# Performance work log

Measured on AMD Instinct MI355X. Metric: run time of the kernel, lower is better.

## Reference

```python
import jax, jax.numpy as jnp
import numpy as np

N_HEADS = 8
TOP_K = 2
EPS = 1e-5


def cross_node(x4, nf, tkv, Wq, bq, Wk, bk, Wv, bv, Wo, bo, gamma, beta, token_mask):
    # x4: [N, BL, 1, D]; nf: [N, BL, K, D]; tkv: [N, K, 1]; token_mask: [N] float (routed subset)
    N, BL, _, D = x4.shape
    K = nf.shape[2]
    H = N_HEADS
    dh = D // H
    nf = nf * tkv[:, None, :, :]  # use_weights: scale neighbors by topk similarity weights
    xf = x4.reshape(N * BL, D)
    nff = nf.reshape(N * BL, K, D)
    q = (xf @ Wq.T + bq).reshape(N * BL, H, dh)
    k = (nff @ Wk.T + bk).reshape(N * BL, K, H, dh)
    v = (nff @ Wv.T + bv).reshape(N * BL, K, H, dh)
    # flash_attn_func math: scaled dot-product over the K neighbors, per head
    scores = jnp.einsum('thd,tkhd->thk', q, k) / jnp.sqrt(jnp.asarray(dh, xf.dtype))
    attn = jax.nn.softmax(scores, axis=-1)
    o = jnp.einsum('thk,tkhd->thd', attn, v).reshape(N * BL, D)
    o = o @ Wo.T + bo
    # masked BatchNorm1d (training-mode batch stats over ONLY the gathered/routed tokens,
    # matching torch where each expert sees just its subset)
    m = jnp.broadcast_to(token_mask[:, None], (N, BL)).reshape(-1, 1)
    cnt = jnp.maximum(m.sum(), 1.0)
    mean = (o * m).sum(0) / cnt
    var = (((o - mean) ** 2) * m).sum(0) / cnt
    o = (o - mean) / jnp.sqrt(var + EPS) * gamma + beta
    return (o + xf).reshape(N, BL, D)


def moe_forward(x, mm, topk_values, Wr, br, eWq, eWk, eWv, eWo, ebq, ebk, ebv, ebo,
                eGamma, eBeta, eW1, eb1, mWq, mWk, mWv, mWo, mbq, mbk, mbv, mbo,
                mGamma, mBeta, mW2, mb2, topk_indices, modality_index):
    N, B, L, D = x.shape
    BL = B * L
    K = topk_indices.shape[1]
    E = Wr.shape[0]
    Mn = mWq.shape[0]
    # neighbor gather: nf[n, b*l, k] = x[topk_indices[n, k], b, l]
    nf = jnp.transpose(x[topk_indices], (0, 2, 3, 1, 4)).reshape(N, BL, K, D)
    x4 = x.reshape(N, BL, 1, D)
    tkv = topk_values.reshape(N, K, 1)
    # router softmax gating
    gate = jax.nn.softmax(mm.reshape(N, D) @ Wr.T + br, axis=-1)  # [N, E]
    _, te = jax.lax.top_k(gate, TOP_K)
    routed = jax.nn.one_hot(te, E, dtype=gate.dtype).sum(1)  # [N, E] 0/1
    f_i = routed.sum(0) / N
    P_i = gate.sum(0) / N
    balance_loss = E * jnp.sum(f_i * P_i)
    # capacity limiting via running cumsum per expert column
    keep = jnp.cumsum(routed, axis=0) <= (N / E)
    rprobs = gate * jnp.where(keep, routed, jnp.zeros_like(routed))
    active = rprobs.sum(-1) > 0  # [N]
    eprobs, eidx = jax.lax.top_k(rprobs, TOP_K)  # [N, TOP_K]
    # expert dispatch/combine (dense-masked equivalent of the per-expert gather/scatter)
    out_tok = jnp.zeros((N, BL, D), x.dtype)
    for i in range(E):
        sel = (eidx == i).any(-1) & active  # tokens gathered for expert i
        mask_f = sel.astype(x.dtype)
        prob_i = (eprobs * (eidx == i)).sum(-1)  # combine weight (0 for capacity-dropped)
        co = cross_node(x4, nf, tkv, eWq[i], ebq[i], eWk[i], ebk[i], eWv[i], ebv[i],
                        eWo[i], ebo[i], eGamma[i], eBeta[i], mask_f)
        co = co @ eW1[i].T + eb1[i]
        out_tok = out_tok + (mask_f * prob_i)[:, None, None] * co
    # modality experts: every token with modality m goes through modality expert m
    mod_out = jnp.zeros_like(out_tok)
    for m in range(Mn):
        mask_f = (modality_index[:, m, :] == 1).any(-1).astype(x.dtype)
        co = cross_node(x4, nf, tkv, mWq[m], mbq[m], mWk[m], mbk[m], mWv[m], mbv[m],
                        mWo[m], mbo[m], mGamma[m], mBeta[m], mask_f)
        co = co @ mW2[m].T + mb2[m]
        mod_out = mod_out + mask_f[:, None, None] * co
    out = (out_tok + mod_out / Mn).reshape(N, B, L, D)
    return out, balance_loss


def setup_inputs():
    key = jax.random.key(0)
    ks = jax.random.split(key, 7)
    N, B, L, D, K, E, Mn = 1024, 2, 8, 128, 16, 4, 4
    s = 1.0 / float(np.sqrt(D))
    inp = {}
    inp['x'] = jax.random.normal(ks[0], (N, B, L, D), jnp.float32)
    inp['mm'] = jax.random.normal(ks[1], (N, 1, D), jnp.float32)
    inp['topk_values'] = jax.random.uniform(ks[2], (N, K), jnp.float32)
    inp['topk_indices'] = jax.random.randint(ks[3], (N, K), 0, N, dtype=jnp.int32)
    inp['modality_index'] = jax.nn.one_hot(
        jax.random.randint(ks[4], (N,), 0, Mn, dtype=jnp.int32), Mn, dtype=jnp.int32
    ).reshape(N, Mn, 1)
    inp['Wr'] = jax.random.normal(ks[5], (E, D), jnp.float32) * s
    inp['br'] = jnp.zeros((E,), jnp.float32)
    kk = jax.random.split(ks[6], 10)
    for j, nm in enumerate(['eWq', 'eWk', 'eWv', 'eWo', 'eW1']):
        inp[nm] = jax.random.normal(kk[j], (E, D, D), jnp.float32) * s
    for j, nm in enumerate(['mWq', 'mWk', 'mWv', 'mWo', 'mW2']):
        inp[nm] = jax.random.normal(kk[5 + j], (Mn, D, D), jnp.float32) * s
    for nm in ['ebq', 'ebk', 'ebv', 'ebo', 'eBeta', 'eb1']:
        inp[nm] = jnp.zeros((E, D), jnp.float32)
    for nm in ['mbq', 'mbk', 'mbv', 'mbo', 'mBeta', 'mb2']:
        inp[nm] = jnp.zeros((Mn, D), jnp.float32)
    inp['eGamma'] = jnp.ones((E, D), jnp.float32)
    inp['mGamma'] = jnp.ones((Mn, D), jnp.float32)
    return inp


def reference(x, mm, topk_values, topk_indices, modality_index, Wr, br,
              eWq, eWk, eWv, eWo, ebq, ebk, ebv, ebo, eGamma, eBeta, eW1, eb1,
              mWq, mWk, mWv, mWo, mbq, mbk, mbv, mbo, mGamma, mBeta, mW2, mb2):
    return moe_forward(x, mm, topk_values, Wr, br, eWq, eWk, eWv, eWo, ebq, ebk, ebv, ebo,
                       eGamma, eBeta, eW1, eb1, mWq, mWk, mWv, mWo, mbq, mbk, mbv, mbo,
                       mGamma, mBeta, mW2, mb2, topk_indices, modality_index)
```

## Files before the change

kernel.cpp:

```cpp
#include <hip/hip_runtime.h>

typedef unsigned short u16;
typedef unsigned int u32;
typedef short short8 __attribute__((ext_vector_type(8)));
typedef float f32x4 __attribute__((ext_vector_type(4)));

#define NTOK 1024
#define TT 16384
#define DD 128
#define EPSV 1e-5f
#define ST 2097152
#define STKV 4194304

__device__ __forceinline__ u16 f2bf(float f) {
    u32 u = __float_as_uint(f);
    u += 0x7fffu + ((u >> 16) & 1u);
    return (u16)(u >> 16);
}
__device__ __forceinline__ u32 pack2(u16 a, u16 b) { return (u32)a | ((u32)b << 16); }
__device__ __forceinline__ void up2(u32 w, float& lo, float& hi) {
    lo = __uint_as_float(w << 16);
    hi = __uint_as_float(w & 0xffff0000u);
}

__global__ __launch_bounds__(256) void k_prep(const float* __restrict__ x,
        const float* __restrict__ eWq, const float* __restrict__ eWk,
        const float* __restrict__ eWv, const float* __restrict__ eWo, const float* __restrict__ eW1,
        const float* __restrict__ mWq, const float* __restrict__ mWk, const float* __restrict__ mWv,
        const float* __restrict__ mWo, const float* __restrict__ mW2,
        const float* __restrict__ mm, const float* __restrict__ Wr, const float* __restrict__ br,
        u16* __restrict__ Xb, u16* __restrict__ Wb, float* __restrict__ logits) {
    int bid = blockIdx.x; int tid = threadIdx.x;
    if (bid < 1024) {
        int i = bid * 256 + tid;
        const float4* p = (const float4*)x + (size_t)i * 2;
        float4 a = p[0], b = p[1];
        uint4 o;
        o.x = pack2(f2bf(a.x), f2bf(a.y));
        o.y = pack2(f2bf(a.z), f2bf(a.w));
        o.z = pack2(f2bf(b.x), f2bf(b.y));
        o.w = pack2(f2bf(b.z), f2bf(b.w));
        *((uint4*)Xb + i) = o;
    } else if (bid < 1344) {
        int i = (bid - 1024) * 256 + tid;
        int tns = i >> 13;
        int off = (i & 8191) * 8;
        const float* src;
        switch (tns) {
            case 0: src = eWq; break; case 1: src = eWk; break; case 2: src = eWv; break;
            case 3: src = eWo; break; case 4: src = eW1; break; case 5: src = mWq; break;
            case 6: src = mWk; break; case 7: src = mWv; break; case 8: src = mWo; break;
            default: src = mW2; break;
        }
        const float4* p = (const float4*)(src + off);
        float4 a = p[0], b = p[1];
        uint4 o;
        o.x = pack2(f2bf(a.x), f2bf(a.y));
        o.y = pack2(f2bf(a.z), f2bf(a.w));
        o.z = pack2(f2bf(b.x), f2bf(b.y));
        o.w = pack2(f2bf(b.z), f2bf(b.w));
        *(uint4*)(Wb + tns * 65536 + off) = o;
    } else {
        int i = (bid - 1344) * 256 + tid;
        int n = i >> 2, e = i & 3;
        const float4* a = (const float4*)(mm + (size_t)n * DD);
        const float4* w = (const float4*)(Wr + (size_t)e * DD);
        float s = 0.f;
#pragma unroll
        for (int j = 0; j < 32; j++) {
            float4 av = a[j], wv = w[j];
            s += av.x * wv.x + av.y * wv.y + av.z * wv.z + av.w * wv.w;
        }
        logits[i] = s + br[e];
    }
}

__global__ __launch_bounds__(1024) void k_route(const float* __restrict__ logits, const int* __restrict__ modix,
                                                float* __restrict__ mask8, float* __restrict__ comb8,
                                                float* __restrict__ cnt8, float* __restrict__ bnsum,
                                                float* __restrict__ bnsq, float* __restrict__ loss) {
    __shared__ int wsum[4][16];
    __shared__ float red[16];
    int n = threadIdx.x;
    if (n < 16) red[n] = 0.f;
    bnsum[n] = 0.f; bnsq[n] = 0.f;
    float g[4];
    float mx = -1e30f;
#pragma unroll
    for (int e = 0; e < 4; e++) { g[e] = logits[n * 4 + e]; mx = fmaxf(mx, g[e]); }
    float s = 0.f;
#pragma unroll
    for (int e = 0; e < 4; e++) { g[e] = expf(g[e] - mx); s += g[e]; }
    float inv = 1.f / s;
#pragma unroll
    for (int e = 0; e < 4; e++) g[e] *= inv;
    int i0 = 0; float b0 = g[0];
#pragma unroll
    for (int e = 1; e < 4; e++) if (g[e] > b0) { b0 = g[e]; i0 = e; }
    int i1 = -1; float b1v = -1e30f;
#pragma unroll
    for (int e = 0; e < 4; e++) if (e != i0 && g[e] > b1v) { b1v = g[e]; i1 = e; }
    u32 rbits = (1u << i0) | (1u << i1);
    int wav = n >> 6, lane = n & 63;
    unsigned long long lm = (~0ull) >> (63 - lane);
    int pre[4];
#pragma unroll
    for (int e = 0; e < 4; e++) {
        unsigned long long m = __ballot((rbits >> e) & 1u);
        pre[e] = __popcll(m & lm);
        if (lane == 63) wsum[e][wav] = __popcll(m);
    }
    __syncthreads();
    float rp[4]; float rsum = 0.f;
#pragma unroll
    for (int e = 0; e < 4; e++) {
        int off = 0;
        for (int w = 0; w < 16; w++) if (w < wav) off += wsum[e][w];
        bool keep = (off + pre[e]) <= 256;
        rp[e] = (((rbits >> e) & 1u) && keep) ? g[e] : 0.f;
        rsum += rp[e];
    }
    bool active = rsum > 0.f;
    int j0 = 0; float c0 = rp[0];
#pragma unroll
    for (int e = 1; e < 4; e++) if (rp[e] > c0) { c0 = rp[e]; j0 = e; }
    int j1 = -1; float c1 = -1e30f;
#pragma unroll
    for (int e = 0; e < 4; e++) if (e != j0 && rp[e] > c1) { c1 = rp[e]; j1 = e; }
    float vals[16];
#pragma unroll
    for (int e = 0; e < 4; e++) {
        bool sel = active && (e == j0 || e == j1);
        float mf = sel ? 1.f : 0.f;
        mask8[e * NTOK + n] = mf;
        comb8[e * NTOK + n] = rp[e];
        vals[e] = mf;
    }
#pragma unroll
    for (int m = 0; m < 4; m++) {
        float mf = (modix[n * 4 + m] == 1) ? 1.f : 0.f;
        mask8[(4 + m) * NTOK + n] = mf;
        comb8[(4 + m) * NTOK + n] = 0.25f * mf;
        vals[4 + m] = mf;
    }
#pragma unroll
    for (int e = 0; e < 4; e++) vals[8 + e] = ((rbits >> e) & 1u) ? 1.f : 0.f;
#pragma unroll
    for (int e = 0; e < 4; e++) vals[12 + e] = g[e];
#pragma unroll
    for (int q = 0; q < 16; q++) {
        float v = vals[q];
        for (int off = 32; off; off >>= 1) v += __shfl_down(v, off, 64);
        if (lane == 0) atomicAdd(&red[q], v);
    }
    __syncthreads();
    if (n == 0) {
        for (int c = 0; c < 8; c++) cnt8[c] = fmaxf(16.f * red[c], 1.f);
        float l = 0.f;
        for (int e = 0; e < 4; e++) l += (red[8 + e] / 1024.f) * (red[12 + e] / 1024.f);
        loss[0] = 4.f * l;
    }
}

__global__ __launch_bounds__(256) void k_gemm_qkv(const u16* __restrict__ Xb, const u16* __restrict__ Wb,
        const float* __restrict__ ebq, const float* __restrict__ mbq,
        const float* __restrict__ mask8,
        u16* __restrict__ Qb, u16* __restrict__ KVb) {
    __shared__ u16 As[64 * 128];
    __shared__ u16 Bs[128 * 128];
    int tid = threadIdx.x; int bm = blockIdx.x; int c = blockIdx.y;
    int wq = (c < 4) ? c : 20 + (c - 4);
    int wk = (c < 4) ? 4 + c : 24 + (c - 4);
    int wv = (c < 4) ? 8 + c : 28 + (c - 4);
    const u16* Wsl[3] = { Wb + wq * 16384, Wb + wk * 16384, Wb + wv * 16384 };
    const float* bq = (c < 4) ? (ebq + c * 128) : (mbq + (c - 4) * 128);
    const float* maskp = mask8 + c * NTOK;
    bool qact = (maskp[bm * 4] != 0.f) || (maskp[bm * 4 + 1] != 0.f) ||
                (maskp[bm * 4 + 2] != 0.f) || (maskp[bm * 4 + 3] != 0.f);
    u16* Qc  = Qb + (size_t)c * ST;
    u16* KVc = KVb + (size_t)c * STKV;

    const uint4* asrc = (const uint4*)(Xb + (size_t)bm * 8192);
#pragma unroll
    for (int it = 0; it < 4; ++it) {
        int ci = it * 256 + tid;
        uint4 v = asrc[ci];
        int byte = ci * 16; int row = byte >> 8;
        *(uint4*)((char*)As + (byte ^ ((row & 7) << 4))) = v;
    }
    __syncthreads();
    int lane = tid & 63, wid = tid >> 6, lr = lane & 15, lg = lane >> 4;
    short8 a[4];
#pragma unroll
    for (int ks = 0; ks < 4; ++ks) {
        int kk = ks * 64 + lg * 16;
        int arow = wid * 16 + lr;
        a[ks] = *(const short8*)((const char*)As + ((arow * 256 + kk) ^ ((arow & 7) << 4)));
    }
    for (int y = 0; y < 3; ++y) {
        if (y == 0 && !qact) continue;
        const uint4* wsrc = (const uint4*)Wsl[y];
#pragma unroll
        for (int it = 0; it < 8; ++it) {
            int qi = it * 256 + tid;
            uint4 v = wsrc[qi];
            int eo = qi * 8; int row = eo >> 7; int byte = eo * 2;
            *(uint4*)((char*)Bs + (byte ^ ((row & 7) << 4))) = v;
        }
        __syncthreads();
        f32x4 acc[8] = {};
#pragma unroll
        for (int ks = 0; ks < 4; ++ks) {
            int kk = ks * 64 + lg * 16;
#pragma unroll
            for (int nc = 0; nc < 8; ++nc) {
                int brow = nc * 16 + lr;
                short8 b = *(const short8*)((const char*)Bs + ((brow * 256 + kk) ^ ((brow & 7) << 4)));
                acc[nc] = __builtin_amdgcn_mfma_f32_16x16x32_bf16(a[ks], b, acc[nc], 0, 0, 0);
            }
        }
        int row0 = bm * 64 + wid * 16 + lg * 4;
#pragma unroll
        for (int nc = 0; nc < 8; ++nc) {
            int col = nc * 16 + lr;
            float bb = (y == 0) ? bq[col] : 0.f;
#pragma unroll
            for (int r = 0; r < 4; r++) {
                u16 hv = f2bf(acc[nc][r] + bb);
                if (y == 0) Qc[(size_t)(row0 + r) * 128 + col] = hv;
                else KVc[(size_t)(row0 + r) * 256 + (y == 2 ? 128 : 0) + col] = hv;
            }
        }
        __syncthreads();
    }
}

__global__ __launch_bounds__(256) void k_attn(const u16* Qb, const u16* __restrict__ KVb,
        const float* __restrict__ tkv, const int* __restrict__ idx,
        const float* __restrict__ ebk, const float* __restrict__ ebv,
        const float* __restrict__ mbk, const float* __restrict__ mbv,
        const float* __restrict__ mask8, u16* Ob) {
    int bid = blockIdx.x;
    int c = bid & 7, inner = bid >> 3;
    int tid = threadIdx.x;
    int gid = inner * 256 + tid;
    int t = gid >> 3, h = gid & 7;
    int n = __builtin_amdgcn_readfirstlane(t >> 4);
    int bl = t & 15;
    if (mask8[c * NTOK + n] == 0.f) return;
    const int4* ip = (const int4*)(idx + n * 16);
    int4 iv0 = ip[0], iv1 = ip[1], iv2 = ip[2], iv3 = ip[3];
    const float4* tp = (const float4*)(tkv + n * 16);
    float4 tv0 = tp[0], tv1 = tp[1], tv2 = tp[2], tv3 = tp[3];
    const u16* Qc = Qb + (size_t)c * ST;
    const u16* KVc = KVb + (size_t)c * STKV;
    u16* Oc = Ob + (size_t)c * ST;
    const float* bk = (c < 4) ? (ebk + c * 128) : (mbk + (c - 4) * 128);
    const float* bv = (c < 4) ? (ebv + c * 128) : (mbv + (c - 4) * 128);
    float qv[16];
    {
        const uint4* qp = (const uint4*)(Qc + (size_t)t * 128 + h * 16);
        uint4 a = qp[0], b = qp[1];
        up2(a.x, qv[0], qv[1]);   up2(a.y, qv[2], qv[3]);
        up2(a.z, qv[4], qv[5]);   up2(a.w, qv[6], qv[7]);
        up2(b.x, qv[8], qv[9]);   up2(b.y, qv[10], qv[11]);
        up2(b.z, qv[12], qv[13]); up2(b.w, qv[14], qv[15]);
    }
    float qb = 0.f;
#pragma unroll
    for (int i = 0; i < 16; i++) qb += qv[i] * bk[h * 16 + i];
    int gsav[16] = { iv0.x, iv0.y, iv0.z, iv0.w, iv1.x, iv1.y, iv1.z, iv1.w,
                     iv2.x, iv2.y, iv2.z, iv2.w, iv3.x, iv3.y, iv3.z, iv3.w };
    float tsav[16] = { tv0.x, tv0.y, tv0.z, tv0.w, tv1.x, tv1.y, tv1.z, tv1.w,
                       tv2.x, tv2.y, tv2.z, tv2.w, tv3.x, tv3.y, tv3.z, tv3.w };
    float scv[16]; float smax = -1e30f;
#pragma unroll 2
    for (int k = 0; k < 16; k++) {
        const uint4* kp = (const uint4*)(KVc + (size_t)(gsav[k] * 16 + bl) * 256 + h * 16);
        uint4 a = kp[0], b = kp[1];
        float d0 = 0.f, d1 = 0.f, lo, hi;
        up2(a.x, lo, hi); d0 = fmaf(lo, qv[0], d0);  d1 = fmaf(hi, qv[1], d1);
        up2(a.y, lo, hi); d0 = fmaf(lo, qv[2], d0);  d1 = fmaf(hi, qv[3], d1);
        up2(a.z, lo, hi); d0 = fmaf(lo, qv[4], d0);  d1 = fmaf(hi, qv[5], d1);
        up2(a.w, lo, hi); d0 = fmaf(lo, qv[6], d0);  d1 = fmaf(hi, qv[7], d1);
        up2(b.x, lo, hi); d0 = fmaf(lo, qv[8], d0);  d1 = fmaf(hi, qv[9], d1);
        up2(b.y, lo, hi); d0 = fmaf(lo, qv[10], d0); d1 = fmaf(hi, qv[11], d1);
        up2(b.z, lo, hi); d0 = fmaf(lo, qv[12], d0); d1 = fmaf(hi, qv[13], d1);
        up2(b.w, lo, hi); d0 = fmaf(lo, qv[14], d0); d1 = fmaf(hi, qv[15], d1);
        float sv = 0.25f * (tsav[k] * (d0 + d1) + qb);
        scv[k] = sv; smax = fmaxf(smax, sv);
    }
    float sum = 0.f;
#pragma unroll
    for (int k = 0; k < 16; k++) { scv[k] = __expf(scv[k] - smax); sum += scv[k]; }
    float inv = 1.f / sum;
    float o[16];
#pragma unroll
    for (int i = 0; i < 16; i++) o[i] = 0.f;
#pragma unroll 2
    for (int k = 0; k < 16; k++) {
        const uint4* vp = (const uint4*)(KVc + (size_t)(gsav[k] * 16 + bl) * 256 + 128 + h * 16);
        uint4 a = vp[0], b = vp[1];
        float cc = scv[k] * inv * tsav[k];
        float lo, hi;
        up2(a.x, lo, hi); o[0] = fmaf(lo, cc, o[0]);   o[1] = fmaf(hi, cc, o[1]);
        up2(a.y, lo, hi); o[2] = fmaf(lo, cc, o[2]);   o[3] = fmaf(hi, cc, o[3]);
        up2(a.z, lo, hi); o[4] = fmaf(lo, cc, o[4]);   o[5] = fmaf(hi, cc, o[5]);
        up2(a.w, lo, hi); o[6] = fmaf(lo, cc, o[6]);   o[7] = fmaf(hi, cc, o[7]);
        up2(b.x, lo, hi); o[8] = fmaf(lo, cc, o[8]);   o[9] = fmaf(hi, cc, o[9]);
        up2(b.y, lo, hi); o[10] = fmaf(lo, cc, o[10]); o[11] = fmaf(hi, cc, o[11]);
        up2(b.z, lo, hi); o[12] = fmaf(lo, cc, o[12]); o[13] = fmaf(hi, cc, o[13]);
        up2(b.w, lo, hi); o[14] = fmaf(lo, cc, o[14]); o[15] = fmaf(hi, cc, o[15]);
    }
#pragma unroll
    for (int i = 0; i < 16; i++) o[i] += bv[h * 16 + i];
    uint4 s0, s1;
    s0.x = pack2(f2bf(o[0]), f2bf(o[1]));  s0.y = pack2(f2bf(o[2]), f2bf(o[3]));
    s0.z = pack2(f2bf(o[4]), f2bf(o[5]));  s0.w = pack2(f2bf(o[6]), f2bf(o[7]));
    s1.x = pack2(f2bf(o[8]), f2bf(o[9]));  s1.y = pack2(f2bf(o[10]), f2bf(o[11]));
    s1.z = pack2(f2bf(o[12]), f2bf(o[13])); s1.w = pack2(f2bf(o[14]), f2bf(o[15]));
    uint4* op = (uint4*)(Oc + (size_t)t * 128 + h * 16);
    op[0] = s0; op[1] = s1;
}

__global__ __launch_bounds__(256) void k_gemm_o(const u16* __restrict__ Ab, const u16* __restrict__ Wb,
        const float* __restrict__ ebo, const float* __restrict__ mbo,
        u16* __restrict__ O2, const float* __restrict__ mask8,
        float* __restrict__ bnsum, float* __restrict__ bnsq) {
    __shared__ u16 As[64 * 128];
    __shared__ u16 Bs[128 * 128];
    __shared__ float ssum[128], ssq[128];
    int tid = threadIdx.x; int bm = blockIdx.x; int c = blockIdx.y;
    const float* maskp = mask8 + c * NTOK;
    if (maskp[bm * 4] == 0.f && maskp[bm * 4 + 1] == 0.f &&
        maskp[bm * 4 + 2] == 0.f && maskp[bm * 4 + 3] == 0.f) return;
    int wo = (c < 4) ? 12 + c : 32 + (c - 4);
    const u16* Wp = Wb + wo * 16384;
    const float* bo = (c < 4) ? (ebo + c * 128) : (mbo + (c - 4) * 128);
    if (tid < 128) { ssum[tid] = 0.f; ssq[tid] = 0.f; }
    const uint4* asrc = (const uint4*)(Ab + (size_t)c * ST + (size_t)bm * 8192);
#pragma unroll
    for (int it = 0; it < 4; ++it) {
        int ci = it * 256 + tid;
        uint4 v = asrc[ci];
        int byte = ci * 16; int row = byte >> 8;
        *(uint4*)((char*)As + (byte ^ ((row & 7) << 4))) = v;
    }
    const uint4* wsrc = (const uint4*)Wp;
#pragma unroll
    for (int it = 0; it < 8; ++it) {
        int qi = it * 256 + tid;
        uint4 v = wsrc[qi];
        int eo = qi * 8; int row = eo >> 7; int byte = eo * 2;
        *(uint4*)((char*)Bs + (byte ^ ((row & 7) << 4))) = v;
    }
    __syncthreads();
    int lane = tid & 63, wid = tid >> 6, lr = lane & 15, lg = lane >> 4;
    f32x4 acc[8] = {};
#pragma unroll
    for (int ks = 0; ks < 4; ++ks) {
        int kk = ks * 64 + lg * 16;
        int arow = wid * 16 + lr;
        short8 a = *(const short8*)((const char*)As + ((arow * 256 + kk) ^ ((arow & 7) << 4)));
#pragma unroll
        for (int nc = 0; nc < 8; ++nc) {
            int brow = nc * 16 + lr;
            short8 b = *(const short8*)((const char*)Bs + ((brow * 256 + kk) ^ ((brow & 7) << 4)));
            acc[nc] = __builtin_amdgcn_mfma_f32_16x16x32_bf16(a, b, acc[nc], 0, 0, 0);
        }
    }
    int nidx = bm * 4 + wid;
    float mk = maskp[nidx];
    int row0 = bm * 64 + wid * 16 + lg * 4;
    u16* O2c = O2 + (size_t)c * ST;
    float ps[8], pq[8];
#pragma unroll
    for (int nc = 0; nc < 8; ++nc) {
        int col = nc * 16 + lr;
        float bb = bo[col];
        float sv = 0.f, qv = 0.f;
#pragma unroll
        for (int r = 0; r < 4; r++) {
            float v = acc[nc][r] + bb;
            if (mk != 0.f) O2c[(size_t)(row0 + r) * 128 + col] = f2bf(v);
            sv += v; qv += v * v;
        }
        ps[nc] = sv * mk; pq[nc] = qv * mk;
    }
#pragma unroll
    for (int nc = 0; nc < 8; ++nc) {
        ps[nc] += __shfl_xor(ps[nc], 16, 64); ps[nc] += __shfl_xor(ps[nc], 32, 64);
        pq[nc] += __shfl_xor(pq[nc], 16, 64); pq[nc] += __shfl_xor(pq[nc], 32, 64);
    }
    if (lane < 16) {
#pragma unroll
        for (int nc = 0; nc < 8; ++nc) {
            atomicAdd(&ssum[nc * 16 + lane], ps[nc]);
            atomicAdd(&ssq[nc * 16 + lane], pq[nc]);
        }
    }
    __syncthreads();
    if (tid < 128) { atomicAdd(&bnsum[c * 128 + tid], ssum[tid]); atomicAdd(&bnsq[c * 128 + tid], ssq[tid]); }
}

__global__ __launch_bounds__(512) void k_gemm_w1(const u16* __restrict__ O2, const u16* __restrict__ Xb,
        const u16* __restrict__ Wb, const float* __restrict__ eb1, const float* __restrict__ mb2,
        const float* __restrict__ eGamma, const float* __restrict__ mGamma,
        const float* __restrict__ eBeta, const float* __restrict__ mBeta,
        const float* __restrict__ comb8, const float* __restrict__ cnt8,
        const float* __restrict__ bnsum, const float* __restrict__ bnsq,
        float* __restrict__ out) {
    __shared__ u16 As[64 * 128];
    __shared__ u16 Bs[128 * 128];
    __shared__ float scall[8][128], shall[8][128];
    int tid = threadIdx.x; int bm = blockIdx.x;
#pragma unroll
    for (int j = 0; j < 2; ++j) {
        int id = j * 512 + tid;
        int c = id >> 7, d = id & 127;
        float cnt = cnt8[c];
        float mean = bnsum[c * 128 + d] / cnt;
        float var = bnsq[c * 128 + d] / cnt - mean * mean;
        float rs = rsqrtf(var + EPSV);
        const float* ga = (c < 4) ? (eGamma + c * 128) : (mGamma + (c - 4) * 128);
        const float* be = (c < 4) ? (eBeta + c * 128) : (mBeta + (c - 4) * 128);
        float gg = ga[d];
        scall[c][d] = rs * gg;
        shall[c][d] = be[d] - mean * rs * gg;
    }
    __syncthreads();
    int lane = tid & 63, wid = tid >> 6, lr = lane & 15, lg = lane >> 4;
    int wm = wid & 3, wn = wid >> 2;
    f32x4 acc[4] = {};
    const uint4* xsrc = (const uint4*)(Xb + (size_t)bm * 8192);
    for (int c = 0; c < 8; ++c) {
        float wc4[4];
        wc4[0] = comb8[c * NTOK + bm * 4];     wc4[1] = comb8[c * NTOK + bm * 4 + 1];
        wc4[2] = comb8[c * NTOK + bm * 4 + 2]; wc4[3] = comb8[c * NTOK + bm * 4 + 3];
        if (wc4[0] == 0.f && wc4[1] == 0.f && wc4[2] == 0.f && wc4[3] == 0.f) continue;
        int wsl = (c < 4) ? 16 + c : 36 + (c - 4);
        const u16* Wp = Wb + wsl * 16384;
        const uint4* osrc = (const uint4*)(O2 + (size_t)c * ST + (size_t)bm * 8192);
#pragma unroll
        for (int it = 0; it < 2; ++it) {
            int qi = it * 512 + tid;
            int eo = qi * 8; int row = eo >> 7; int cb = eo & 127;
            float wc = wc4[row >> 4];
            uint4 ov = osrc[qi]; uint4 xv = xsrc[qi];
            float olo, ohi, xlo, xhi;
            uint4 hh;
            up2(ov.x, olo, ohi); up2(xv.x, xlo, xhi);
            hh.x = pack2(f2bf((olo * scall[c][cb] + shall[c][cb] + xlo) * wc),
                         f2bf((ohi * scall[c][cb + 1] + shall[c][cb + 1] + xhi) * wc));
            up2(ov.y, olo, ohi); up2(xv.y, xlo, xhi);
            hh.y = pack2(f2bf((olo * scall[c][cb + 2] + shall[c][cb + 2] + xlo) * wc),
                         f2bf((ohi * scall[c][cb + 3] + shall[c][cb + 3] + xhi) * wc));
            up2(ov.z, olo, ohi); up2(xv.z, xlo, xhi);
            hh.z = pack2(f2bf((olo * scall[c][cb + 4] + shall[c][cb + 4] + xlo) * wc),
                         f2bf((ohi * scall[c][cb + 5] + shall[c][cb + 5] + xhi) * wc));
            up2(ov.w, olo, ohi); up2(xv.w, xlo, xhi);
            hh.w = pack2(f2bf((olo * scall[c][cb + 6] + shall[c][cb + 6] + xlo) * wc),
                         f2bf((ohi * scall[c][cb + 7] + shall[c][cb + 7] + xhi) * wc));
            *(uint4*)((char*)As + ((eo * 2) ^ ((row & 7) << 4))) = hh;
        }
        const uint4* wsrc = (const uint4*)Wp;
#pragma unroll
        for (int it = 0; it < 4; ++it) {
            int qi = it * 512 + tid;
            uint4 v = wsrc[qi];
            int eo = qi * 8; int row = eo >> 7; int byte = eo * 2;
            *(uint4*)((char*)Bs + (byte ^ ((row & 7) << 4))) = v;
        }
        __syncthreads();
#pragma unroll
        for (int ks = 0; ks < 4; ++ks) {
            int kk = ks * 64 + lg * 16;
            int arow = wm * 16 + lr;
            short8 a = *(const short8*)((const char*)As + ((arow * 256 + kk) ^ ((arow & 7) << 4)));
#pragma unroll
            for (int nc = 0; nc < 4; ++nc) {
                int brow = wn * 64 + nc * 16 + lr;
                short8 b = *(const short8*)((const char*)Bs + ((brow * 256 + kk) ^ ((brow & 7) << 4)));
                acc[nc] = __builtin_amdgcn_mfma_f32_16x16x32_bf16(a, b, acc[nc], 0, 0, 0);
            }
        }
        __syncthreads();
    }
    int nidx = bm * 4 + wm;
    int row0 = bm * 64 + wm * 16 + lg * 4;
    float wc8[8];
#pragma unroll
    for (int c = 0; c < 8; ++c) wc8[c] = comb8[c * NTOK + nidx];
#pragma unroll
    for (int nc = 0; nc < 4; ++nc) {
        int col = wn * 64 + nc * 16 + lr;
        float bias = 0.f;
#pragma unroll
        for (int c = 0; c < 8; ++c) {
            const float* b1 = (c < 4) ? (eb1 + c * 128) : (mb2 + (c - 4) * 128);
            bias += wc8[c] * b1[col];
        }
#pragma unroll
        for (int r = 0; r < 4; r++)
            out[(size_t)(row0 + r) * 128 + col] = acc[nc][r] + bias;
    }
}

extern "C" void kernel_launch(void* const* d_in, const int* in_sizes, int n_in,
                              void* d_out, int out_size, void* d_ws, size_t ws_size,
                              hipStream_t stream) {
    (void)in_sizes; (void)n_in; (void)ws_size; (void)out_size;
    const float* x    = (const float*)d_in[0];
    const float* mm   = (const float*)d_in[1];
    const float* tkv  = (const float*)d_in[2];
    const int*   idx  = (const int*)d_in[3];
    const int*   modi = (const int*)d_in[4];
    const float* Wr   = (const float*)d_in[5];
    const float* br   = (const float*)d_in[6];
    const float* eWq = (const float*)d_in[7],  *eWk = (const float*)d_in[8],  *eWv = (const float*)d_in[9];
    const float* eWo = (const float*)d_in[10], *eW1 = (const float*)d_in[11];
    const float* mWq = (const float*)d_in[12], *mWk = (const float*)d_in[13], *mWv = (const float*)d_in[14];
    const float* mWo = (const float*)d_in[15], *mW2 = (const float*)d_in[16];
    const float* ebq = (const float*)d_in[17], *ebk = (const float*)d_in[18], *ebv = (const float*)d_in[19];
    const float* ebo = (const float*)d_in[20], *eBeta = (const float*)d_in[21], *eb1 = (const float*)d_in[22];
    const float* mbq = (const float*)d_in[23], *mbk = (const float*)d_in[24], *mbv = (const float*)d_in[25];
    const float* mbo = (const float*)d_in[26], *mBeta = (const float*)d_in[27], *mb2 = (const float*)d_in[28];
    const float* eGamma = (const float*)d_in[29], *mGamma = (const float*)d_in[30];
    float* out = (float*)d_out;

    char* wsb = (char*)d_ws;
    const size_t MB = 1024 * 1024;
    u16* Xb  = (u16*)wsb;
    u16* Wb  = (u16*)(wsb + 4 * MB);
    u16* Qb  = (u16*)(wsb + 8 * MB);
    u16* KVb = (u16*)(wsb + 40 * MB);
    u16* O2  = (u16*)(wsb + 104 * MB);
    float* logits = (float*)(wsb + 136 * MB);
    float* comb8 = logits + 4096;
    float* mask8 = comb8 + 8192;
    float* cnt8  = mask8 + 8192;
    float* bnsum = cnt8 + 16;
    float* bnsq  = bnsum + 1024;

    k_prep<<<1360, 256, 0, stream>>>(x, eWq, eWk, eWv, eWo, eW1, mWq, mWk, mWv, mWo, mW2,
                                     mm, Wr, br, Xb, Wb, logits);
    k_route<<<1, 1024, 0, stream>>>(logits, modi, mask8, comb8, cnt8, bnsum, bnsq,
                                    out + (size_t)TT * DD);
    k_gemm_qkv<<<dim3(256, 8), 256, 0, stream>>>(Xb, Wb, ebq, mbq, mask8, Qb, KVb);
    k_attn<<<4096, 256, 0, stream>>>(Qb, KVb, tkv, idx, ebk, ebv, mbk, mbv, mask8, Qb);
    k_gemm_o<<<dim3(256, 8), 256, 0, stream>>>(Qb, Wb, ebo, mbo, O2, mask8, bnsum, bnsq);
    k_gemm_w1<<<256, 512, 0, stream>>>(O2, Xb, Wb, eb1, mb2, eGamma, mGamma, eBeta, mBeta,
                                       comb8, cnt8, bnsum, bnsq, out);
}
```

Measured before the change: 117.8 us.

## Fuse router into prep kernel and raise attention loop unroll

Merges the separate single-block routing kernel into the prep kernel as its last block, computing router logits per token in registers instead of through a global logits buffer. This removes one kernel launch and its serialization. Prep blocks grow to 1024 threads. The attention K/V loops are also unrolled by 4 instead of 2 to raise memory-level parallelism, at the cost of more registers.

```diff
diff --git a/kernel.cpp b/kernel.cpp
--- a/kernel.cpp
+++ b/kernel.cpp
@@ -23,16 +23,19 @@
     hi = __uint_as_float(w & 0xffff0000u);
 }
 
-__global__ __launch_bounds__(256) void k_prep(const float* __restrict__ x,
+__global__ __launch_bounds__(1024) void k_prep(const float* __restrict__ x,
         const float* __restrict__ eWq, const float* __restrict__ eWk,
         const float* __restrict__ eWv, const float* __restrict__ eWo, const float* __restrict__ eW1,
         const float* __restrict__ mWq, const float* __restrict__ mWk, const float* __restrict__ mWv,
         const float* __restrict__ mWo, const float* __restrict__ mW2,
         const float* __restrict__ mm, const float* __restrict__ Wr, const float* __restrict__ br,
-        u16* __restrict__ Xb, u16* __restrict__ Wb, float* __restrict__ logits) {
+        const int* __restrict__ modix,
+        u16* __restrict__ Xb, u16* __restrict__ Wb,
+        float* __restrict__ mask8, float* __restrict__ comb8, float* __restrict__ cnt8,
+        float* __restrict__ bnsum, float* __restrict__ bnsq, float* __restrict__ loss) {
     int bid = blockIdx.x; int tid = threadIdx.x;
-    if (bid < 1024) {
-        int i = bid * 256 + tid;
+    if (bid < 256) {
+        int i = bid * 1024 + tid;
         const float4* p = (const float4*)x + (size_t)i * 2;
         float4 a = p[0], b = p[1];
         uint4 o;
@@ -41,8 +44,10 @@
         o.z = pack2(f2bf(b.x), f2bf(b.y));
         o.w = pack2(f2bf(b.z), f2bf(b.w));
         *((uint4*)Xb + i) = o;
-    } else if (bid < 1344) {
-        int i = (bid - 1024) * 256 + tid;
+        return;
+    }
+    if (bid < 336) {
+        int i = (bid - 256) * 1024 + tid;
         int tns = i >> 13;
         int off = (i & 8191) * 8;
         const float* src;
@@ -60,34 +65,34 @@
         o.z = pack2(f2bf(b.x), f2bf(b.y));
         o.w = pack2(f2bf(b.z), f2bf(b.w));
         *(uint4*)(Wb + tns * 65536 + off) = o;
-    } else {
-        int i = (bid - 1344) * 256 + tid;
-        int n = i >> 2, e = i & 3;
-        const float4* a = (const float4*)(mm + (size_t)n * DD);
-        const float4* w = (const float4*)(Wr + (size_t)e * DD);
-        float s = 0.f;
-#pragma unroll
-        for (int j = 0; j < 32; j++) {
-            float4 av = a[j], wv = w[j];
-            s += av.x * wv.x + av.y * wv.y + av.z * wv.z + av.w * wv.w;
-        }
-        logits[i] = s + br[e];
-    }
-}
-
-__global__ __launch_bounds__(1024) void k_route(const float* __restrict__ logits, const int* __restrict__ modix,
-                                                float* __restrict__ mask8, float* __restrict__ comb8,
-                                                float* __restrict__ cnt8, float* __restrict__ bnsum,
-                                                float* __restrict__ bnsq, float* __restrict__ loss) {
+        return;
+    }
     __shared__ int wsum[4][16];
     __shared__ float red[16];
-    int n = threadIdx.x;
+    int n = tid;
     if (n < 16) red[n] = 0.f;
     bnsum[n] = 0.f; bnsq[n] = 0.f;
     float g[4];
+    {
+        const float4* a = (const float4*)(mm + (size_t)n * DD);
+        float4 av[32];
+#pragma unroll
+        for (int j = 0; j < 32; j++) av[j] = a[j];
+#pragma unroll
+        for (int e = 0; e < 4; e++) {
+            const float4* w = (const float4*)(Wr + (size_t)e * DD);
+            float s = 0.f;
+#pragma unroll
+            for (int j = 0; j < 32; j++) {
+                float4 wv = w[j];
+                s += av[j].x * wv.x + av[j].y * wv.y + av[j].z * wv.z + av[j].w * wv.w;
+            }
+            g[e] = s + br[e];
+        }
+    }
     float mx = -1e30f;
 #pragma unroll
-    for (int e = 0; e < 4; e++) { g[e] = logits[n * 4 + e]; mx = fmaxf(mx, g[e]); }
+    for (int e = 0; e < 4; e++) mx = fmaxf(mx, g[e]);
     float s = 0.f;
 #pragma unroll
     for (int e = 0; e < 4; e++) { g[e] = expf(g[e] - mx); s += g[e]; }
@@ -274,7 +279,7 @@
     float tsav[16] = { tv0.x, tv0.y, tv0.z, tv0.w, tv1.x, tv1.y, tv1.z, tv1.w,
                        tv2.x, tv2.y, tv2.z, tv2.w, tv3.x, tv3.y, tv3.z, tv3.w };
     float scv[16]; float smax = -1e30f;
-#pragma unroll 2
+#pragma unroll 4
     for (int k = 0; k < 16; k++) {
         const uint4* kp = (const uint4*)(KVc + (size_t)(gsav[k] * 16 + bl) * 256 + h * 16);
         uint4 a = kp[0], b = kp[1];
@@ -297,7 +302,7 @@
     float o[16];
 #pragma unroll
     for (int i = 0; i < 16; i++) o[i] = 0.f;
-#pragma unroll 2
+#pragma unroll 4
     for (int k = 0; k < 16; k++) {
         const uint4* vp = (const uint4*)(KVc + (size_t)(gsav[k] * 16 + bl) * 256 + 128 + h * 16);
         uint4 a = vp[0], b = vp[1];
@@ -535,17 +540,15 @@
     u16* Qb  = (u16*)(wsb + 8 * MB);
     u16* KVb = (u16*)(wsb + 40 * MB);
     u16* O2  = (u16*)(wsb + 104 * MB);
-    float* logits = (float*)(wsb + 136 * MB);
-    float* comb8 = logits + 4096;
+    float* comb8 = (float*)(wsb + 136 * MB);
     float* mask8 = comb8 + 8192;
     float* cnt8  = mask8 + 8192;
     float* bnsum = cnt8 + 16;
     float* bnsq  = bnsum + 1024;
 
-    k_prep<<<1360, 256, 0, stream>>>(x, eWq, eWk, eWv, eWo, eW1, mWq, mWk, mWv, mWo, mW2,
-                                     mm, Wr, br, Xb, Wb, logits);
-    k_route<<<1, 1024, 0, stream>>>(logits, modi, mask8, comb8, cnt8, bnsum, bnsq,
-                                    out + (size_t)TT * DD);
+    k_prep<<<337, 1024, 0, stream>>>(x, eWq, eWk, eWv, eWo, eW1, mWq, mWk, mWv, mWo, mW2,
+                                     mm, Wr, br, modi, Xb, Wb,
+                                     mask8, comb8, cnt8, bnsum, bnsq, out + (size_t)TT * DD);
     k_gemm_qkv<<<dim3(256, 8), 256, 0, stream>>>(Xb, Wb, ebq, mbq, mask8, Qb, KVb);
     k_attn<<<4096, 256, 0, stream>>>(Qb, KVb, tkv, idx, ebk, ebv, mbk, mbv, mask8, Qb);
     k_gemm_o<<<dim3(256, 8), 256, 0, stream>>>(Qb, Wb, ebo, mbo, O2, mask8, bnsum, bnsq);
```

Result: slower. 131.0 us (+11.2%).
